# Optimization experiments

Hardware: AMD Instinct MI355X
Metric: run time of the kernel (lower is better)

Reference implementation:

```python
import jax, jax.numpy as jnp
import numpy as np


def setup_inputs() -> dict:
    key = jax.random.key(0)
    k1, k2, k3 = jax.random.split(key, 3)
    B, H, S, D = 2, 16, 2048, 64
    return {
        "q": jax.random.normal(k1, (B, H, S, D), dtype=jnp.float32),
        "k": jax.random.normal(k2, (B, H, S, D), dtype=jnp.float32),
        "v": jax.random.normal(k3, (B, H, S, D), dtype=jnp.float32),
        "chunk_size": 256,
    }


def reference(q, k, v, chunk_size):
    # Chunked Based linear attention: linear (K^T V) + rank-3 quadratic (K x K x V)
    # inter-chunk state recurrence (shifted/exclusive cumsum over chunks) plus the
    # intra-chunk causal part with kernel  s = q.k;  phi = s + 0.5*s^2.
    B, H, S, D = q.shape
    C = chunk_size
    N = S // C
    scale = D ** (-0.5)

    qc = (q * scale).reshape(B, H, N, C, D)
    kc = k.reshape(B, H, N, C, D)
    vc = v.reshape(B, H, N, C, D)

    # ---- linear inter-chunk state: shifted cumsum of K^T V per chunk ----
    KV = jnp.einsum("bhncd,bhnce->bhnde", kc, vc)            # (B,H,N,D,D)
    S_lin = jnp.cumsum(KV, axis=2) - KV                       # exclusive cumsum
    o_lin = jnp.einsum("bhncd,bhnde->bhnce", qc, S_lin)

    # ---- quadratic inter-chunk state: shifted cumsum of sum_c K_d K_e V_f ----
    KKV = jnp.einsum("bhncd,bhnce,bhncf->bhndef", kc, kc, vc)  # (B,H,N,D,D,D)
    S_quad = jnp.cumsum(KKV, axis=2) - KKV                     # exclusive cumsum
    o_quad = 0.5 * jnp.einsum("bhndef,bhncd,bhnce->bhncf", S_quad, qc, qc)

    # ---- intra-chunk causal quadratic attention ----
    A = jnp.einsum("bhncd,bhnmd->bhncm", qc, kc)               # (B,H,N,C,C)
    mask = jnp.tril(jnp.ones((C, C), dtype=bool))
    Ak = jnp.where(mask, A + 0.5 * A * A, 0.0)
    o_intra = jnp.einsum("bhncm,bhnmf->bhncf", Ak, vc)

    out = (o_lin + o_quad + o_intra).reshape(B, H, S, D)
    return out
```

## Files before the change

### kernel.cpp

```cpp
#include <hip/hip_runtime.h>
#include <stdint.h>

#define SEQ  2048
#define DH   64
#define BH_N 32
#define SCALE 0.125f

typedef __attribute__((ext_vector_type(8))) short short8;
typedef __attribute__((ext_vector_type(4))) float f32x4;

static __device__ __forceinline__ unsigned short f2bf(float f) {
  unsigned int u = __float_as_uint(f);
  u += 0x7fffu + ((u >> 16) & 1u);
  return (unsigned short)(u >> 16);
}
static __device__ __forceinline__ unsigned cvtpk(float a, float b) {
  unsigned r;
  asm("v_cvt_pk_bf16_f32 %0, %1, %2" : "=v"(r) : "v"(a), "v"(b));
  return r;
}

__global__ __launch_bounds__(256) void prep_kernel(
    const float* __restrict__ kin, const float* __restrict__ vin,
    unsigned short* __restrict__ kb2, unsigned short* __restrict__ vt2)
{
  const int sb = blockIdx.x;
  const int bh = blockIdx.y;
  const int t  = threadIdx.x;
  __shared__ __align__(16) unsigned short lds[4096];
  const size_t base  = ((size_t)bh * SEQ + (size_t)sb * 64) * DH;
  const size_t obase = ((size_t)bh * 32 + sb) * 4096;

  #pragma unroll
  for (int i = 0; i < 4; ++i) {
    int idx = i * 256 + t, key = idx >> 4, F = (idx & 15) * 4;
    float4 f = *reinterpret_cast<const float4*>(kin + base + key * DH + F);
    int pos = (key & 32) | ((key & 4) << 2) | ((key & 24) >> 1) | (key & 3);
    int c = (F >> 5) * 4 + ((F >> 3) & 3), jh = (F >> 2) & 1;
    uint2 pk; pk.x = cvtpk(f.x, f.y); pk.y = cvtpk(f.z, f.w);
    *reinterpret_cast<uint2*>(lds + (c * 64 + pos) * 8 + jh * 4) = pk;
  }
  __syncthreads();
  #pragma unroll
  for (int uu = 0; uu < 2; ++uu) {
    int u = uu * 256 + t;
    *reinterpret_cast<uint4*>(kb2 + obase + u * 8) =
        *reinterpret_cast<const uint4*>(lds + u * 8);
  }
  __syncthreads();
  #pragma unroll
  for (int i = 0; i < 4; ++i) {
    int idx = i * 256 + t, key = idx >> 4, F = (idx & 15) * 4;
    float4 f = *reinterpret_cast<const float4*>(vin + base + key * DH + F);
    int a = key >> 5, qd = (key >> 3) & 3, jj = key & 7;
    int u0 = a * 256 + (F >> 4) * 64 + qd * 16 + (F & 15);
    lds[(u0 + 0) * 8 + jj] = f2bf(f.x);
    lds[(u0 + 1) * 8 + jj] = f2bf(f.y);
    lds[(u0 + 2) * 8 + jj] = f2bf(f.z);
    lds[(u0 + 3) * 8 + jj] = f2bf(f.w);
  }
  __syncthreads();
  #pragma unroll
  for (int uu = 0; uu < 2; ++uu) {
    int u = uu * 256 + t;
    *reinterpret_cast<uint4*>(vt2 + obase + u * 8) =
        *reinterpret_cast<const uint4*>(lds + u * 8);
  }
}

__global__ __launch_bounds__(256, 2) void attn_kernel(
    const float* __restrict__ q,
    const unsigned short* __restrict__ kb2,
    const unsigned short* __restrict__ vt2,
    float* __restrict__ out)
{
  const int lid  = blockIdx.y * 16 + blockIdx.x;
  const int xcd  = lid & 7;
  const int jj_  = lid >> 3;
  const int bh   = (xcd << 2) | (jj_ >> 4);
  const int qa   = jj_ & 15;
  const int tid  = threadIdx.x;
  const int w    = tid >> 6;
  const int lane = tid & 63;
  const int low  = lane & 15;
  const int quad = lane >> 4;
  const int p    = w >> 1;
  const int rh   = w & 1;
  const int nB   = 32 - qa;

  __shared__ __align__(16) float mls[8192];

  const unsigned short* kb_h = kb2 + (size_t)bh * 32 * 4096;
  const unsigned short* v2_h = vt2 + (size_t)bh * 32 * 4096;

  short8 aqA[2][2], aqB[2][2];
  #pragma unroll
  for (int tsel = 0; tsel < 2; ++tsel) {
    const int qt = tsel ? (31 - qa) : qa;
    #pragma unroll
    for (int h = 0; h < 2; ++h) {
      const float* qp =
          q + ((size_t)bh * SEQ + qt * 64 + rh * 32 + h * 16 + low) * DH + quad * 8;
      #pragma unroll
      for (int ks = 0; ks < 2; ++ks) {
        float4 f0 = *reinterpret_cast<const float4*>(qp + ks * 32);
        float4 f1 = *reinterpret_cast<const float4*>(qp + ks * 32 + 4);
        uint4 uv;
        uv.x = cvtpk(f0.x * SCALE, f0.y * SCALE);
        uv.y = cvtpk(f0.z * SCALE, f0.w * SCALE);
        uv.z = cvtpk(f1.x * SCALE, f1.y * SCALE);
        uv.w = cvtpk(f1.z * SCALE, f1.w * SCALE);
        short8 a = __builtin_bit_cast(short8, uv);
        if (tsel) aqB[h][ks] = a; else aqA[h][ks] = a;
      }
    }
  }

  f32x4 oaccA[2][4], oaccB[2][4];
  #pragma unroll
  for (int h = 0; h < 2; ++h)
    #pragma unroll
    for (int i = 0; i < 4; ++i) {
      oaccA[h][i] = (f32x4){0.f, 0.f, 0.f, 0.f};
      oaccB[h][i] = (f32x4){0.f, 0.f, 0.f, 0.f};
    }

  #define PRELOADG(T, A, KB, VB)                                               \
    do {                                                                       \
      const unsigned short* kTg_ = kb_h + (size_t)(T) * 4096;                  \
      const unsigned short* vTg_ = v2_h + (size_t)(T) * 4096;                  \
      _Pragma("unroll")                                                        \
      for (int ft = 0; ft < 4; ++ft)                                           \
        VB[ft] = *reinterpret_cast<const short8*>(                             \
            vTg_ + (((A) * 4 + ft) * 64 + lane) * 8);                          \
      _Pragma("unroll")                                                        \
      for (int ks = 0; ks < 2; ++ks) {                                         \
        KB[ks * 2 + 0] = *reinterpret_cast<const short8*>(                     \
            kTg_ + ((ks * 4 + quad) * 64 + ((A) * 2 + 0) * 16 + low) * 8);     \
        KB[ks * 2 + 1] = *reinterpret_cast<const short8*>(                     \
            kTg_ + ((ks * 4 + quad) * 64 + ((A) * 2 + 1) * 16 + low) * 8);     \
      }                                                                        \
    } while (0)

  #define COMPUTEG(KB, VB, A, AQ, OACC)                                        \
    do {                                                                       \
      f32x4 s00 = (f32x4){0.f, 0.f, 0.f, 0.f};                                 \
      f32x4 s01 = s00, s10 = s00, s11 = s00;                                   \
      _Pragma("unroll")                                                        \
      for (int ks = 0; ks < 2; ++ks) {                                         \
        s00 = __builtin_amdgcn_mfma_f32_16x16x32_bf16(                         \
            KB[ks * 2 + 0], AQ[0][ks], s00, 0, 0, 0);                          \
        s01 = __builtin_amdgcn_mfma_f32_16x16x32_bf16(                         \
            KB[ks * 2 + 0], AQ[1][ks], s01, 0, 0, 0);                          \
        s10 = __builtin_amdgcn_mfma_f32_16x16x32_bf16(                         \
            KB[ks * 2 + 1], AQ[0][ks], s10, 0, 0, 0);                          \
        s11 = __builtin_amdgcn_mfma_f32_16x16x32_bf16(                         \
            KB[ks * 2 + 1], AQ[1][ks], s11, 0, 0, 0);                          \
      }                                                                        \
      _Pragma("unroll")                                                        \
      for (int h = 0; h < 2; ++h) {                                            \
        f32x4 sA = h ? s01 : s00;                    \
        f32x4 sB = h ? s11 : s10;                    \
        float pv[8];                                                           \
        _Pragma("unroll")                                                      \
        for (int r = 0; r < 4; ++r) {                                          \
          float x0 = sA[r], x1 = sB[r];                                        \
          pv[r]     = __builtin_fmaf(0.5f * x0, x0, x0);                       \
          pv[4 + r] = __builtin_fmaf(0.5f * x1, x1, x1);                       \
        }                                                                      \
        if (diag) {                                                            \
          const int qrow = rh * 32 + h * 16 + low;                             \
          _Pragma("unroll")                                                    \
          for (int r = 0; r < 4; ++r) {                                        \
            if (((A) * 32 + quad * 8 + r) > qrow)     pv[r]     = 0.f;         \
            if (((A) * 32 + quad * 8 + 4 + r) > qrow) pv[4 + r] = 0.f;         \
          }                                                                    \
        }                                                                      \
        uint4 uu;                                                              \
        uu.x = cvtpk(pv[0], pv[1]); uu.y = cvtpk(pv[2], pv[3]);                \
        uu.z = cvtpk(pv[4], pv[5]); uu.w = cvtpk(pv[6], pv[7]);                \
        short8 pf = __builtin_bit_cast(short8, uu);                            \
        _Pragma("unroll")                                                      \
        for (int ft = 0; ft < 4; ++ft)                                         \
          OACC[h][ft] = __builtin_amdgcn_mfma_f32_16x16x32_bf16(               \
              VB[ft], pf, OACC[h][ft], 0, 0, 0);                               \
      }                                                                        \
    } while (0)

  short8 k0f[4], v0f[4], k1f[4], v1f[4];
  {
    const int T0 = (p < nB) ? p : (p - nB);
    PRELOADG(T0, 0, k0f, v0f);
    PRELOADG(T0, 1, k1f, v1f);
  }
  for (int s = p; s <= 32; s += 2) {
    int sn = s + 2; if (sn > 32) sn = 32;
    const int Tn = (sn < nB) ? sn : (sn - nB);
    const bool diag = (s == nB - 1) || (s == 32);
    if (s >= nB) COMPUTEG(k0f, v0f, 0, aqA, oaccA);
    else         COMPUTEG(k0f, v0f, 0, aqB, oaccB);
    PRELOADG(Tn, 0, k0f, v0f);
    if (s >= nB) COMPUTEG(k1f, v1f, 1, aqA, oaccA);
    else         COMPUTEG(k1f, v1f, 1, aqB, oaccB);
    PRELOADG(Tn, 1, k1f, v1f);
  }

  __syncthreads();
  float* mw = mls + rh * 4096;
  if (p == 1) {
    #pragma unroll
    for (int h = 0; h < 2; ++h)
      #pragma unroll
      for (int ft = 0; ft < 4; ++ft) {
        *reinterpret_cast<f32x4*>(mw + ((0 * 8 + h * 4 + ft) * 256 + lane * 4)) =
            oaccA[h][ft];
        *reinterpret_cast<f32x4*>(mw + ((1 * 8 + h * 4 + ft) * 256 + lane * 4)) =
            oaccB[h][ft];
      }
  }
  __syncthreads();
  if (p == 0) {
    #pragma unroll
    for (int tsel = 0; tsel < 2; ++tsel) {
      const int qt = tsel ? (31 - qa) : qa;
      #pragma unroll
      for (int h = 0; h < 2; ++h)
        #pragma unroll
        for (int ft = 0; ft < 4; ++ft) {
          f32x4 o = tsel ? oaccB[h][ft] : oaccA[h][ft];
          f32x4 m = *reinterpret_cast<const f32x4*>(
              mw + ((tsel * 8 + h * 4 + ft) * 256 + lane * 4));
          o += m;
          *reinterpret_cast<f32x4*>(
              out + ((size_t)bh * SEQ + qt * 64 + rh * 32 + h * 16 + low) * DH +
              ft * 16 + quad * 4) = o;
        }
    }
  }
}

extern "C" void kernel_launch(void* const* d_in, const int* in_sizes, int n_in,
                              void* d_out, int out_size, void* d_ws, size_t ws_size,
                              hipStream_t stream)
{
  const float* q = (const float*)d_in[0];
  const float* k = (const float*)d_in[1];
  const float* v = (const float*)d_in[2];
  float* out = (float*)d_out;

  unsigned short* kb2 = (unsigned short*)d_ws;
  unsigned short* vt2 = kb2 + (size_t)BH_N * SEQ * DH;

  prep_kernel<<<dim3(32, BH_N), 256, 0, stream>>>(k, v, kb2, vt2);
  attn_kernel<<<dim3(16, BH_N), 256, 0, stream>>>(q, kb2, vt2, out);
}
```

Before: 119.1 us.

## Stage K/V tiles through LDS with async global_load_lds ring buffer

Replaces per-wave direct global-to-register K/V fragment loads with a 4-deep LDS ring buffer filled by global_load_lds. Each wave now processes every tile: it splits by key sub-block instead of by alternating tiles, and reads fragments from LDS after a barrier each iteration. MFMA sections are wrapped in s_setprio raises. The aim is to cut duplicated global traffic and hide latency through asynchronous prefetch two tiles ahead. In exchange it adds a block-wide barrier per tile, 64KB of LDS (which may limit occupancy to 2 blocks), and relies on a hand-written vmcnt wait count being correct.

```diff
diff --git a/kernel.cpp b/kernel.cpp
--- a/kernel.cpp
+++ b/kernel.cpp
@@ -18,6 +18,12 @@
   unsigned r;
   asm("v_cvt_pk_bf16_f32 %0, %1, %2" : "=v"(r) : "v"(a), "v"(b));
   return r;
+}
+
+typedef __attribute__((address_space(1))) const unsigned char* gp1;
+typedef __attribute__((address_space(3))) unsigned char* lp3;
+static __device__ __forceinline__ void stage16(const void* g, void* l) {
+  __builtin_amdgcn_global_load_lds((gp1)g, (lp3)l, 16, 0, 0);
 }
 
 __global__ __launch_bounds__(256) void prep_kernel(
@@ -84,11 +90,12 @@
   const int lane = tid & 63;
   const int low  = lane & 15;
   const int quad = lane >> 4;
-  const int p    = w >> 1;
   const int rh   = w & 1;
+  const int ag   = w >> 1;
   const int nB   = 32 - qa;
 
-  __shared__ __align__(16) float mls[8192];
+  __shared__ __align__(16) unsigned short klsAll[4 * 4096];
+  __shared__ __align__(16) unsigned short vlsAll[4 * 4096];
 
   const unsigned short* kb_h = kb2 + (size_t)bh * 32 * 4096;
   const unsigned short* v2_h = vt2 + (size_t)bh * 32 * 4096;
@@ -125,42 +132,53 @@
       oaccB[h][i] = (f32x4){0.f, 0.f, 0.f, 0.f};
     }
 
-  #define PRELOADG(T, A, KB, VB)                                               \
+  const int stV   = w >> 1;
+  const int half_ = w & 1;
+  const unsigned short* gsrc = stV ? v2_h : kb_h;
+  unsigned short* ldsb = stV ? vlsAll : klsAll;
+
+  #define STAGE(T, BUF)                                                        \
     do {                                                                       \
-      const unsigned short* kTg_ = kb_h + (size_t)(T) * 4096;                  \
-      const unsigned short* vTg_ = v2_h + (size_t)(T) * 4096;                  \
-      _Pragma("unroll")                                                        \
-      for (int ft = 0; ft < 4; ++ft)                                           \
-        VB[ft] = *reinterpret_cast<const short8*>(                             \
-            vTg_ + (((A) * 4 + ft) * 64 + lane) * 8);                          \
-      _Pragma("unroll")                                                        \
-      for (int ks = 0; ks < 2; ++ks) {                                         \
-        KB[ks * 2 + 0] = *reinterpret_cast<const short8*>(                     \
-            kTg_ + ((ks * 4 + quad) * 64 + ((A) * 2 + 0) * 16 + low) * 8);     \
-        KB[ks * 2 + 1] = *reinterpret_cast<const short8*>(                     \
-            kTg_ + ((ks * 4 + quad) * 64 + ((A) * 2 + 1) * 16 + low) * 8);     \
+      const unsigned short* gs_ = gsrc + (size_t)(T) * 4096;                   \
+      unsigned short* ld_ = ldsb + (BUF) * 4096;                               \
+      _Pragma("unroll")                                                        \
+      for (int r_ = 0; r_ < 4; ++r_) {                                         \
+        const int u_ = (half_ * 4 + r_) * 64 + lane;                           \
+        stage16(gs_ + u_ * 8, ld_ + u_ * 8);                                   \
       }                                                                        \
     } while (0)
 
-  #define COMPUTEG(KB, VB, A, AQ, OACC)                                        \
+  #define COMPUTE(AQ, OACC)                                                    \
     do {                                                                       \
+      short8 vfr[4], kfr[4];                                                   \
+      _Pragma("unroll")                                                        \
+      for (int ft = 0; ft < 4; ++ft)                                           \
+        vfr[ft] = *reinterpret_cast<const short8*>(                            \
+            vT + ((ag * 4 + ft) * 64 + lane) * 8);                             \
+      _Pragma("unroll")                                                        \
+      for (int ks = 0; ks < 2; ++ks)                                           \
+        _Pragma("unroll")                                                      \
+        for (int sub = 0; sub < 2; ++sub)                                      \
+          kfr[ks * 2 + sub] = *reinterpret_cast<const short8*>(                \
+              kT + ((ks * 4 + quad) * 64 + (ag * 2 + sub) * 16 + low) * 8);    \
       f32x4 s00 = (f32x4){0.f, 0.f, 0.f, 0.f};                                 \
       f32x4 s01 = s00, s10 = s00, s11 = s00;                                   \
+      __builtin_amdgcn_s_setprio(1);                                           \
       _Pragma("unroll")                                                        \
       for (int ks = 0; ks < 2; ++ks) {                                         \
         s00 = __builtin_amdgcn_mfma_f32_16x16x32_bf16(                         \
-            KB[ks * 2 + 0], AQ[0][ks], s00, 0, 0, 0);                          \
+            kfr[ks * 2 + 0], AQ[0][ks], s00, 0, 0, 0);                         \
         s01 = __builtin_amdgcn_mfma_f32_16x16x32_bf16(                         \
-            KB[ks * 2 + 0], AQ[1][ks], s01, 0, 0, 0);                          \
+            kfr[ks * 2 + 0], AQ[1][ks], s01, 0, 0, 0);                         \
         s10 = __builtin_amdgcn_mfma_f32_16x16x32_bf16(                         \
-            KB[ks * 2 + 1], AQ[0][ks], s10, 0, 0, 0);                          \
+            kfr[ks * 2 + 1], AQ[0][ks], s10, 0, 0, 0);                         \
         s11 = __builtin_amdgcn_mfma_f32_16x16x32_bf16(                         \
-            KB[ks * 2 + 1], AQ[1][ks], s11, 0, 0, 0);                          \
+            kfr[ks * 2 + 1], AQ[1][ks], s11, 0, 0, 0);                         \
       }                                                                        \
       _Pragma("unroll")                                                        \
       for (int h = 0; h < 2; ++h) {                                            \
-        f32x4 sA = h ? s01 : s00;                    \
-        f32x4 sB = h ? s11 : s10;                    \
+        f32x4 sA = h ? s01 : s00;                   \
+        f32x4 sB = h ? s11 : s10;                   \
         float pv[8];                                                           \
         _Pragma("unroll")                                                      \
         for (int r = 0; r < 4; ++r) {                                          \
@@ -172,8 +190,8 @@
           const int qrow = rh * 32 + h * 16 + low;                             \
           _Pragma("unroll")                                                    \
           for (int r = 0; r < 4; ++r) {                                        \
-            if (((A) * 32 + quad * 8 + r) > qrow)     pv[r]     = 0.f;         \
-            if (((A) * 32 + quad * 8 + 4 + r) > qrow) pv[4 + r] = 0.f;         \
+            if ((ag * 32 + quad * 8 + r) > qrow)     pv[r]     = 0.f;          \
+            if ((ag * 32 + quad * 8 + 4 + r) > qrow) pv[4 + r] = 0.f;          \
           }                                                                    \
         }                                                                      \
         uint4 uu;                                                              \
@@ -183,31 +201,34 @@
         _Pragma("unroll")                                                      \
         for (int ft = 0; ft < 4; ++ft)                                         \
           OACC[h][ft] = __builtin_amdgcn_mfma_f32_16x16x32_bf16(               \
-              VB[ft], pf, OACC[h][ft], 0, 0, 0);                               \
+              vfr[ft], pf, OACC[h][ft], 0, 0, 0);                             \
       }                                                                        \
+      __builtin_amdgcn_s_setprio(0);                                           \
     } while (0)
 
-  short8 k0f[4], v0f[4], k1f[4], v1f[4];
-  {
-    const int T0 = (p < nB) ? p : (p - nB);
-    PRELOADG(T0, 0, k0f, v0f);
-    PRELOADG(T0, 1, k1f, v1f);
-  }
-  for (int s = p; s <= 32; s += 2) {
-    int sn = s + 2; if (sn > 32) sn = 32;
-    const int Tn = (sn < nB) ? sn : (sn - nB);
+  STAGE(0, 0);
+  STAGE(1, 1);
+
+  for (int s = 0; s <= 32; ++s) {
+    int sp = s + 2; if (sp > 32) sp = 32;
+    const int Tp = (sp < nB) ? sp : (sp - nB);
+    STAGE(Tp, (s + 2) & 3);
+    asm volatile("s_waitcnt vmcnt(8)" ::: "memory");
+    __builtin_amdgcn_s_barrier();
+    asm volatile("" ::: "memory");
+
+    const int buf = s & 3;
+    const unsigned short* kT = klsAll + buf * 4096;
+    const unsigned short* vT = vlsAll + buf * 4096;
     const bool diag = (s == nB - 1) || (s == 32);
-    if (s >= nB) COMPUTEG(k0f, v0f, 0, aqA, oaccA);
-    else         COMPUTEG(k0f, v0f, 0, aqB, oaccB);
-    PRELOADG(Tn, 0, k0f, v0f);
-    if (s >= nB) COMPUTEG(k1f, v1f, 1, aqA, oaccA);
-    else         COMPUTEG(k1f, v1f, 1, aqB, oaccB);
-    PRELOADG(Tn, 1, k1f, v1f);
-  }
-
-  __syncthreads();
-  float* mw = mls + rh * 4096;
-  if (p == 1) {
+    if (s >= nB) COMPUTE(aqA, oaccA);
+    else         COMPUTE(aqB, oaccB);
+  }
+
+  __syncthreads();
+  float* mls = reinterpret_cast<float*>(&klsAll[0]);
+  float* mw  = mls + rh * 4096;
+  if (ag == 1) {
     #pragma unroll
     for (int h = 0; h < 2; ++h)
       #pragma unroll
@@ -219,7 +240,7 @@
       }
   }
   __syncthreads();
-  if (p == 0) {
+  if (ag == 0) {
     #pragma unroll
     for (int tsel = 0; tsel < 2; ++tsel) {
       const int qt = tsel ? (31 - qa) : qa;
```

Result: no change. 121.0 us (+1.6%).

## Assign one query tile per block, split key half-tiles across wave pairs

Applied to the files above, without the earlier changes.

The kernel previously paired query tiles qa and 31-qa in one block for load balance, with wave pairs taking alternating key tiles. Now each block handles a single 64-row query tile, scheduled longest-first (qt = 31 - j>>2), and the two wave pairs split each key tile into 32-key halves. This doubles the grid to 1024 blocks, raises launch bounds to 3 blocks per CU, halves accumulator registers and shared memory, and uses a simpler double-buffered loop. The trade-off is uneven per-block work, which relies on the descending scheduling order and higher occupancy to smooth it out.

```diff
diff --git a/kernel.cpp b/kernel.cpp
--- a/kernel.cpp
+++ b/kernel.cpp
@@ -68,99 +68,90 @@
   }
 }
 
-__global__ __launch_bounds__(256, 2) void attn_kernel(
+__global__ __launch_bounds__(256, 3) void attn_kernel(
     const float* __restrict__ q,
     const unsigned short* __restrict__ kb2,
     const unsigned short* __restrict__ vt2,
     float* __restrict__ out)
 {
-  const int lid  = blockIdx.y * 16 + blockIdx.x;
+  const int lid  = blockIdx.y * 32 + blockIdx.x;
   const int xcd  = lid & 7;
-  const int jj_  = lid >> 3;
-  const int bh   = (xcd << 2) | (jj_ >> 4);
-  const int qa   = jj_ & 15;
+  const int j    = lid >> 3;
+  const int bh   = (xcd << 2) | (j & 3);
+  const int qt   = 31 - (j >> 2);
   const int tid  = threadIdx.x;
   const int w    = tid >> 6;
   const int lane = tid & 63;
   const int low  = lane & 15;
   const int quad = lane >> 4;
-  const int p    = w >> 1;
   const int rh   = w & 1;
-  const int nB   = 32 - qa;
-
-  __shared__ __align__(16) float mls[8192];
+  const int ag   = w >> 1;
+
+  __shared__ __align__(16) float mls[4096];
 
   const unsigned short* kb_h = kb2 + (size_t)bh * 32 * 4096;
   const unsigned short* v2_h = vt2 + (size_t)bh * 32 * 4096;
 
-  short8 aqA[2][2], aqB[2][2];
-  #pragma unroll
-  for (int tsel = 0; tsel < 2; ++tsel) {
-    const int qt = tsel ? (31 - qa) : qa;
-    #pragma unroll
-    for (int h = 0; h < 2; ++h) {
-      const float* qp =
-          q + ((size_t)bh * SEQ + qt * 64 + rh * 32 + h * 16 + low) * DH + quad * 8;
-      #pragma unroll
-      for (int ks = 0; ks < 2; ++ks) {
-        float4 f0 = *reinterpret_cast<const float4*>(qp + ks * 32);
-        float4 f1 = *reinterpret_cast<const float4*>(qp + ks * 32 + 4);
-        uint4 uv;
-        uv.x = cvtpk(f0.x * SCALE, f0.y * SCALE);
-        uv.y = cvtpk(f0.z * SCALE, f0.w * SCALE);
-        uv.z = cvtpk(f1.x * SCALE, f1.y * SCALE);
-        uv.w = cvtpk(f1.z * SCALE, f1.w * SCALE);
-        short8 a = __builtin_bit_cast(short8, uv);
-        if (tsel) aqB[h][ks] = a; else aqA[h][ks] = a;
-      }
+  short8 aq[2][2];
+  #pragma unroll
+  for (int h = 0; h < 2; ++h) {
+    const float* qp =
+        q + ((size_t)bh * SEQ + qt * 64 + rh * 32 + h * 16 + low) * DH + quad * 8;
+    #pragma unroll
+    for (int ks = 0; ks < 2; ++ks) {
+      float4 f0 = *reinterpret_cast<const float4*>(qp + ks * 32);
+      float4 f1 = *reinterpret_cast<const float4*>(qp + ks * 32 + 4);
+      uint4 uv;
+      uv.x = cvtpk(f0.x * SCALE, f0.y * SCALE);
+      uv.y = cvtpk(f0.z * SCALE, f0.w * SCALE);
+      uv.z = cvtpk(f1.x * SCALE, f1.y * SCALE);
+      uv.w = cvtpk(f1.z * SCALE, f1.w * SCALE);
+      aq[h][ks] = __builtin_bit_cast(short8, uv);
     }
   }
 
-  f32x4 oaccA[2][4], oaccB[2][4];
+  f32x4 oacc[2][4];
   #pragma unroll
   for (int h = 0; h < 2; ++h)
     #pragma unroll
-    for (int i = 0; i < 4; ++i) {
-      oaccA[h][i] = (f32x4){0.f, 0.f, 0.f, 0.f};
-      oaccB[h][i] = (f32x4){0.f, 0.f, 0.f, 0.f};
-    }
-
-  #define PRELOADG(T, A, KB, VB)                                               \
+    for (int i = 0; i < 4; ++i)
+      oacc[h][i] = (f32x4){0.f, 0.f, 0.f, 0.f};
+
+  #define PRELOADQ(T, KB, VB)                                                  \
     do {                                                                       \
       const unsigned short* kTg_ = kb_h + (size_t)(T) * 4096;                  \
       const unsigned short* vTg_ = v2_h + (size_t)(T) * 4096;                  \
       _Pragma("unroll")                                                        \
       for (int ft = 0; ft < 4; ++ft)                                           \
         VB[ft] = *reinterpret_cast<const short8*>(                             \
-            vTg_ + (((A) * 4 + ft) * 64 + lane) * 8);                          \
-      _Pragma("unroll")                                                        \
-      for (int ks = 0; ks < 2; ++ks) {                                         \
-        KB[ks * 2 + 0] = *reinterpret_cast<const short8*>(                     \
-            kTg_ + ((ks * 4 + quad) * 64 + ((A) * 2 + 0) * 16 + low) * 8);     \
-        KB[ks * 2 + 1] = *reinterpret_cast<const short8*>(                     \
-            kTg_ + ((ks * 4 + quad) * 64 + ((A) * 2 + 1) * 16 + low) * 8);     \
-      }                                                                        \
+            vTg_ + ((ag * 4 + ft) * 64 + lane) * 8);                           \
+      _Pragma("unroll")                                                        \
+      for (int ks = 0; ks < 2; ++ks)                                           \
+        _Pragma("unroll")                                                      \
+        for (int sub = 0; sub < 2; ++sub)                                      \
+          KB[ks * 2 + sub] = *reinterpret_cast<const short8*>(                 \
+              kTg_ + ((ks * 4 + quad) * 64 + (ag * 2 + sub) * 16 + low) * 8);  \
     } while (0)
 
-  #define COMPUTEG(KB, VB, A, AQ, OACC)                                        \
+  #define COMPUTEQ(KB, VB)                                                     \
     do {                                                                       \
       f32x4 s00 = (f32x4){0.f, 0.f, 0.f, 0.f};                                 \
       f32x4 s01 = s00, s10 = s00, s11 = s00;                                   \
       _Pragma("unroll")                                                        \
       for (int ks = 0; ks < 2; ++ks) {                                         \
         s00 = __builtin_amdgcn_mfma_f32_16x16x32_bf16(                         \
-            KB[ks * 2 + 0], AQ[0][ks], s00, 0, 0, 0);                          \
+            KB[ks * 2 + 0], aq[0][ks], s00, 0, 0, 0);                          \
         s01 = __builtin_amdgcn_mfma_f32_16x16x32_bf16(                         \
-            KB[ks * 2 + 0], AQ[1][ks], s01, 0, 0, 0);                          \
+            KB[ks * 2 + 0], aq[1][ks], s01, 0, 0, 0);                          \
         s10 = __builtin_amdgcn_mfma_f32_16x16x32_bf16(                         \
-            KB[ks * 2 + 1], AQ[0][ks], s10, 0, 0, 0);                          \
+            KB[ks * 2 + 1], aq[0][ks], s10, 0, 0, 0);                          \
         s11 = __builtin_amdgcn_mfma_f32_16x16x32_bf16(                         \
-            KB[ks * 2 + 1], AQ[1][ks], s11, 0, 0, 0);                          \
+            KB[ks * 2 + 1], aq[1][ks], s11, 0, 0, 0);                          \
       }                                                                        \
       _Pragma("unroll")                                                        \
       for (int h = 0; h < 2; ++h) {                                            \
-        f32x4 sA = h ? s01 : s00;                    \
-        f32x4 sB = h ? s11 : s10;                    \
+        f32x4 sA = h ? s01 : s00;                   \
+        f32x4 sB = h ? s11 : s10;                   \
         float pv[8];                                                           \
         _Pragma("unroll")                                                      \
         for (int r = 0; r < 4; ++r) {                                          \
@@ -172,8 +163,8 @@
           const int qrow = rh * 32 + h * 16 + low;                             \
           _Pragma("unroll")                                                    \
           for (int r = 0; r < 4; ++r) {                                        \
-            if (((A) * 32 + quad * 8 + r) > qrow)     pv[r]     = 0.f;         \
-            if (((A) * 32 + quad * 8 + 4 + r) > qrow) pv[4 + r] = 0.f;         \
+            if ((ag * 32 + quad * 8 + r) > qrow)     pv[r]     = 0.f;          \
+            if ((ag * 32 + quad * 8 + 4 + r) > qrow) pv[4 + r] = 0.f;          \
           }                                                                    \
         }                                                                      \
         uint4 uu;                                                              \
@@ -182,60 +173,57 @@
         short8 pf = __builtin_bit_cast(short8, uu);                            \
         _Pragma("unroll")                                                      \
         for (int ft = 0; ft < 4; ++ft)                                         \
-          OACC[h][ft] = __builtin_amdgcn_mfma_f32_16x16x32_bf16(               \
-              VB[ft], pf, OACC[h][ft], 0, 0, 0);                               \
+          oacc[h][ft] = __builtin_amdgcn_mfma_f32_16x16x32_bf16(               \
+              VB[ft], pf, oacc[h][ft], 0, 0, 0);                               \
       }                                                                        \
     } while (0)
 
-  short8 k0f[4], v0f[4], k1f[4], v1f[4];
-  {
-    const int T0 = (p < nB) ? p : (p - nB);
-    PRELOADG(T0, 0, k0f, v0f);
-    PRELOADG(T0, 1, k1f, v1f);
-  }
-  for (int s = p; s <= 32; s += 2) {
-    int sn = s + 2; if (sn > 32) sn = 32;
-    const int Tn = (sn < nB) ? sn : (sn - nB);
-    const bool diag = (s == nB - 1) || (s == 32);
-    if (s >= nB) COMPUTEG(k0f, v0f, 0, aqA, oaccA);
-    else         COMPUTEG(k0f, v0f, 0, aqB, oaccB);
-    PRELOADG(Tn, 0, k0f, v0f);
-    if (s >= nB) COMPUTEG(k1f, v1f, 1, aqA, oaccA);
-    else         COMPUTEG(k1f, v1f, 1, aqB, oaccB);
-    PRELOADG(Tn, 1, k1f, v1f);
-  }
-
-  __syncthreads();
-  float* mw = mls + rh * 4096;
-  if (p == 1) {
+  short8 kA[4], vA[4], kB[4], vB[4];
+  PRELOADQ(0, kA, vA);
+  int s = 0;
+  for (;;) {
+    {
+      int sn = s + 1; if (sn > qt) sn = qt;
+      PRELOADQ(sn, kB, vB);
+      const bool diag = (s == qt);
+      COMPUTEQ(kA, vA);
+      if (s == qt) break;
+      ++s;
+    }
+    {
+      int sn = s + 1; if (sn > qt) sn = qt;
+      PRELOADQ(sn, kA, vA);
+      const bool diag = (s == qt);
+      COMPUTEQ(kB, vB);
+      if (s == qt) break;
+      ++s;
+    }
+  }
+
+  __syncthreads();
+  float* mw = mls + rh * 2048;
+  if (ag == 1) {
+    #pragma unroll
+    for (int h = 0; h < 2; ++h)
+      #pragma unroll
+      for (int ft = 0; ft < 4; ++ft)
+        *reinterpret_cast<f32x4*>(mw + ((h * 4 + ft) * 256 + lane * 4)) =
+            oacc[h][ft];
+  }
+  __syncthreads();
+  if (ag == 0) {
     #pragma unroll
     for (int h = 0; h < 2; ++h)
       #pragma unroll
       for (int ft = 0; ft < 4; ++ft) {
-        *reinterpret_cast<f32x4*>(mw + ((0 * 8 + h * 4 + ft) * 256 + lane * 4)) =
-            oaccA[h][ft];
-        *reinterpret_cast<f32x4*>(mw + ((1 * 8 + h * 4 + ft) * 256 + lane * 4)) =
-            oaccB[h][ft];
+        f32x4 o = oacc[h][ft];
+        f32x4 m = *reinterpret_cast<const f32x4*>(
+            mw + ((h * 4 + ft) * 256 + lane * 4));
+        o += m;
+        *reinterpret_cast<f32x4*>(
+            out + ((size_t)bh * SEQ + qt * 64 + rh * 32 + h * 16 + low) * DH +
+            ft * 16 + quad * 4) = o;
       }
-  }
-  __syncthreads();
-  if (p == 0) {
-    #pragma unroll
-    for (int tsel = 0; tsel < 2; ++tsel) {
-      const int qt = tsel ? (31 - qa) : qa;
-      #pragma unroll
-      for (int h = 0; h < 2; ++h)
-        #pragma unroll
-        for (int ft = 0; ft < 4; ++ft) {
-          f32x4 o = tsel ? oaccB[h][ft] : oaccA[h][ft];
-          f32x4 m = *reinterpret_cast<const f32x4*>(
-              mw + ((tsel * 8 + h * 4 + ft) * 256 + lane * 4));
-          o += m;
-          *reinterpret_cast<f32x4*>(
-              out + ((size_t)bh * SEQ + qt * 64 + rh * 32 + h * 16 + low) * DH +
-              ft * 16 + quad * 4) = o;
-        }
-    }
   }
 }
 
@@ -252,5 +240,5 @@
   unsigned short* vt2 = kb2 + (size_t)BH_N * SEQ * DH;
 
   prep_kernel<<<dim3(32, BH_N), 256, 0, stream>>>(k, v, kb2, vt2);
-  attn_kernel<<<dim3(16, BH_N), 256, 0, stream>>>(q, kb2, vt2, out);
-}
+  attn_kernel<<<dim3(32, 32), 256, 0, stream>>>(q, kb2, vt2, out);
+}
```

Result: slower. 123.7 us (+3.9%).
